# Kernel optimization log

Measured on AMD Instinct MI355X. Metric: run time of the kernel, lower is better.

Reference implementation:

```python
import jax, jax.numpy as jnp
import numpy as np

EPS = 1e-3  # Q = eps * I(5) in the original module

def setup_inputs() -> dict:
    key = jax.random.key(0)
    k1, k2, k3 = jax.random.split(key, 3)
    B, n = 4194304, 5
    x = jax.random.normal(k1, (B, n), dtype=jnp.float32)
    # fc1 = nn.Linear(n, n): weight [n, n], bias [n]
    W = jax.random.normal(k2, (n, n), dtype=jnp.float32) * (1.0 / np.sqrt(n))
    b_fc = jax.random.normal(k3, (n,), dtype=jnp.float32) * 0.1
    return {"x": x, "W": W, "b_fc": b_fc}

def reference(x, W, b_fc):
    # h = fc1(x)  (the QP inequality RHS per sample)
    h = x @ W.T + b_fc  # [B, 5]
    # Per-sample QP: min_z 0.5*eps*||z||^2 + 1^T z  s.t.  -z <= h  (G = -I)
    # Separable closed form (exact solution cvxopt converges to):
    #   unconstrained minimizer z_i = -1/eps; constraint z_i >= -h_i
    #   => z_i = max(-h_i, -1/eps)
    z = jnp.maximum(-h, -1.0 / EPS)  # [B, 5] primal solutions
    return z
```

## Files before the change

kernel.cpp:

```cpp
#include <hip/hip_runtime.h>


#define BLOCK 256
#define WAVES_PER_BLOCK 4
#define F4_PER_TILE 320
#define TILES_PER_WAVE 4

typedef float vf4 __attribute__((ext_vector_type(4)));

__global__ __launch_bounds__(BLOCK) void qpnet_kernel(
    const float* __restrict__ x,
    const float* __restrict__ W,
    const float* __restrict__ bfc,
    float* __restrict__ out,
    int total_f4)
{
    __shared__ __align__(16) float lds[BLOCK * 20];

    float w[5][5];
    float bias[5];
#pragma unroll
    for (int j = 0; j < 5; ++j) {
        bias[j] = bfc[j];
#pragma unroll
        for (int i = 0; i < 5; ++i) w[j][i] = W[j * 5 + i];
    }

    const int wave = threadIdx.x >> 6;
    const int lane = threadIdx.x & 63;
    float* __restrict__ wlds = &lds[wave * (64 * 20)];

    const int wave_id = blockIdx.x * WAVES_PER_BLOCK + wave;
    int tb = wave_id * (F4_PER_TILE * TILES_PER_WAVE);
    if (tb >= total_f4) return;

    const vf4* __restrict__ xin  = reinterpret_cast<const vf4*>(x);
    vf4* __restrict__       zout = reinterpret_cast<vf4*>(out);

    vf4 r[5];
#pragma unroll
    for (int k = 0; k < 5; ++k) r[k] = xin[tb + k * 64 + lane];

    for (int t = 0; t < TILES_PER_WAVE; ++t) {
        const int cur = tb + t * F4_PER_TILE;
        if (cur >= total_f4) break;

#pragma unroll
        for (int k = 0; k < 5; ++k)
            *reinterpret_cast<vf4*>(&wlds[(k * 64 + lane) * 4]) = r[k];

        const int nxt = cur + F4_PER_TILE;
        if (t + 1 < TILES_PER_WAVE && nxt < total_f4) {
#pragma unroll
            for (int k = 0; k < 5; ++k) r[k] = xin[nxt + k * 64 + lane];
        }

        asm volatile("s_waitcnt lgkmcnt(0)" ::: "memory");

        float v[20];
#pragma unroll
        for (int p = 0; p < 5; ++p)
            *reinterpret_cast<vf4*>(&v[4 * p]) =
                *reinterpret_cast<const vf4*>(&wlds[lane * 20 + 4 * p]);

#pragma unroll
        for (int k = 0; k < 4; ++k) {
            float t0 = bias[0], t1 = bias[1], t2 = bias[2], t3 = bias[3], t4 = bias[4];
#pragma unroll
            for (int i = 0; i < 5; ++i) {
                const float xv = v[k * 5 + i];
                t0 = fmaf(xv, w[0][i], t0);
                t1 = fmaf(xv, w[1][i], t1);
                t2 = fmaf(xv, w[2][i], t2);
                t3 = fmaf(xv, w[3][i], t3);
                t4 = fmaf(xv, w[4][i], t4);
            }
            v[k * 5 + 0] = fmaxf(-t0, -1000.0f);
            v[k * 5 + 1] = fmaxf(-t1, -1000.0f);
            v[k * 5 + 2] = fmaxf(-t2, -1000.0f);
            v[k * 5 + 3] = fmaxf(-t3, -1000.0f);
            v[k * 5 + 4] = fmaxf(-t4, -1000.0f);
        }

#pragma unroll
        for (int p = 0; p < 5; ++p)
            *reinterpret_cast<vf4*>(&wlds[lane * 20 + 4 * p]) =
                *reinterpret_cast<const vf4*>(&v[4 * p]);
        asm volatile("s_waitcnt lgkmcnt(0)" ::: "memory");

#pragma unroll
        for (int k = 0; k < 5; ++k)
            zout[cur + k * 64 + lane] =
                *reinterpret_cast<const vf4*>(&wlds[(k * 64 + lane) * 4]);
    }
}

extern "C" void kernel_launch(void* const* d_in, const int* in_sizes, int n_in,
                              void* d_out, int out_size, void* d_ws, size_t ws_size,
                              hipStream_t stream) {
    const float* x   = (const float*)d_in[0];
    const float* W   = (const float*)d_in[1];
    const float* bfc = (const float*)d_in[2];
    float* out = (float*)d_out;

    int total_f4 = in_sizes[0] / 4;
    int f4_per_wave = F4_PER_TILE * TILES_PER_WAVE;
    int n_waves  = (total_f4 + f4_per_wave - 1) / f4_per_wave;
    int grid     = (n_waves + WAVES_PER_BLOCK - 1) / WAVES_PER_BLOCK;

    qpnet_kernel<<<grid, BLOCK, 0, stream>>>(x, W, bfc, out, total_f4);
}
```

Baseline: 155.6 us.

## Drop LDS transpose and load five contiguous float4 per lane directly

Removes the shared-memory staging that transposed coalesced float4 loads into per-thread 20-float groups. Each lane now reads its own five consecutive float4 straight from global memory, and both tiles are loaded up front before compute instead of being software-pipelined. Tiles per wave drop from four to two, doubling the grid. This removes LDS traffic and waits, but global accesses become strided by 80 bytes across lanes, which may hurt coalescing. Trailing elements not covered by a full 5-float4 group would be skipped, though the test size divides evenly.

```diff
diff --git a/kernel.cpp b/kernel.cpp
--- a/kernel.cpp
+++ b/kernel.cpp
@@ -4,9 +4,42 @@
 #define BLOCK 256
 #define WAVES_PER_BLOCK 4
 #define F4_PER_TILE 320
-#define TILES_PER_WAVE 4
+#define TILES_PER_WAVE 2
 
 typedef float vf4 __attribute__((ext_vector_type(4)));
+
+__device__ __forceinline__ void process4(vf4 a[5], const float w[5][5],
+                                         const float bias[5]) {
+    float v[20];
+#pragma unroll
+    for (int k = 0; k < 5; ++k)
+#pragma unroll
+        for (int c = 0; c < 4; ++c) v[k * 4 + c] = a[k][c];
+
+#pragma unroll
+    for (int r = 0; r < 4; ++r) {
+        float t0 = bias[0], t1 = bias[1], t2 = bias[2], t3 = bias[3], t4 = bias[4];
+#pragma unroll
+        for (int i = 0; i < 5; ++i) {
+            const float xv = v[r * 5 + i];
+            t0 = fmaf(xv, w[0][i], t0);
+            t1 = fmaf(xv, w[1][i], t1);
+            t2 = fmaf(xv, w[2][i], t2);
+            t3 = fmaf(xv, w[3][i], t3);
+            t4 = fmaf(xv, w[4][i], t4);
+        }
+        v[r * 5 + 0] = fmaxf(-t0, -1000.0f);
+        v[r * 5 + 1] = fmaxf(-t1, -1000.0f);
+        v[r * 5 + 2] = fmaxf(-t2, -1000.0f);
+        v[r * 5 + 3] = fmaxf(-t3, -1000.0f);
+        v[r * 5 + 4] = fmaxf(-t4, -1000.0f);
+    }
+
+#pragma unroll
+    for (int k = 0; k < 5; ++k)
+#pragma unroll
+        for (int c = 0; c < 4; ++c) a[k][c] = v[k * 4 + c];
+}
 
 __global__ __launch_bounds__(BLOCK) void qpnet_kernel(
     const float* __restrict__ x,
@@ -15,8 +48,6 @@
     float* __restrict__ out,
     int total_f4)
 {
-    __shared__ __align__(16) float lds[BLOCK * 20];
-
     float w[5][5];
     float bias[5];
 #pragma unroll
@@ -28,70 +59,33 @@
 
     const int wave = threadIdx.x >> 6;
     const int lane = threadIdx.x & 63;
-    float* __restrict__ wlds = &lds[wave * (64 * 20)];
-
     const int wave_id = blockIdx.x * WAVES_PER_BLOCK + wave;
-    int tb = wave_id * (F4_PER_TILE * TILES_PER_WAVE);
-    if (tb >= total_f4) return;
 
     const vf4* __restrict__ xin  = reinterpret_cast<const vf4*>(x);
     vf4* __restrict__       zout = reinterpret_cast<vf4*>(out);
 
-    vf4 r[5];
+    const int base0 = wave_id * (F4_PER_TILE * TILES_PER_WAVE) + lane * 5;
+    const int base1 = base0 + F4_PER_TILE;
+    const bool do0 = (base0 + 5 <= total_f4);
+    const bool do1 = (base1 + 5 <= total_f4);
+    if (!do0) return;
+
+    vf4 a[5], b[5];
 #pragma unroll
-    for (int k = 0; k < 5; ++k) r[k] = xin[tb + k * 64 + lane];
+    for (int k = 0; k < 5; ++k) a[k] = xin[base0 + k];
+    if (do1) {
+#pragma unroll
+        for (int k = 0; k < 5; ++k) b[k] = xin[base1 + k];
+    }
 
-    for (int t = 0; t < TILES_PER_WAVE; ++t) {
-        const int cur = tb + t * F4_PER_TILE;
-        if (cur >= total_f4) break;
+    process4(a, w, bias);
+#pragma unroll
+    for (int k = 0; k < 5; ++k) zout[base0 + k] = a[k];
 
+    if (do1) {
+        process4(b, w, bias);
 #pragma unroll
-        for (int k = 0; k < 5; ++k)
-            *reinterpret_cast<vf4*>(&wlds[(k * 64 + lane) * 4]) = r[k];
-
-        const int nxt = cur + F4_PER_TILE;
-        if (t + 1 < TILES_PER_WAVE && nxt < total_f4) {
-#pragma unroll
-            for (int k = 0; k < 5; ++k) r[k] = xin[nxt + k * 64 + lane];
-        }
-
-        asm volatile("s_waitcnt lgkmcnt(0)" ::: "memory");
-
-        float v[20];
-#pragma unroll
-        for (int p = 0; p < 5; ++p)
-            *reinterpret_cast<vf4*>(&v[4 * p]) =
-                *reinterpret_cast<const vf4*>(&wlds[lane * 20 + 4 * p]);
-
-#pragma unroll
-        for (int k = 0; k < 4; ++k) {
-            float t0 = bias[0], t1 = bias[1], t2 = bias[2], t3 = bias[3], t4 = bias[4];
-#pragma unroll
-            for (int i = 0; i < 5; ++i) {
-                const float xv = v[k * 5 + i];
-                t0 = fmaf(xv, w[0][i], t0);
-                t1 = fmaf(xv, w[1][i], t1);
-                t2 = fmaf(xv, w[2][i], t2);
-                t3 = fmaf(xv, w[3][i], t3);
-                t4 = fmaf(xv, w[4][i], t4);
-            }
-            v[k * 5 + 0] = fmaxf(-t0, -1000.0f);
-            v[k * 5 + 1] = fmaxf(-t1, -1000.0f);
-            v[k * 5 + 2] = fmaxf(-t2, -1000.0f);
-            v[k * 5 + 3] = fmaxf(-t3, -1000.0f);
-            v[k * 5 + 4] = fmaxf(-t4, -1000.0f);
-        }
-
-#pragma unroll
-        for (int p = 0; p < 5; ++p)
-            *reinterpret_cast<vf4*>(&wlds[lane * 20 + 4 * p]) =
-                *reinterpret_cast<const vf4*>(&v[4 * p]);
-        asm volatile("s_waitcnt lgkmcnt(0)" ::: "memory");
-
-#pragma unroll
-        for (int k = 0; k < 5; ++k)
-            zout[cur + k * 64 + lane] =
-                *reinterpret_cast<const vf4*>(&wlds[(k * 64 + lane) * 4]);
+        for (int k = 0; k < 5; ++k) zout[base1 + k] = b[k];
     }
 }
 
```

After: 163.7 us. 1.05x slower.
